# Kernel optimization log

Hardware: AMD Instinct MI355X
Metric: run time of the kernel (lower is better)

## Reference

```python
import jax, jax.numpy as jnp
import numpy as np

B, S, D, H = 2, 2048, 1024, 16
DH = D // H


def setup_inputs() -> dict:
    key = jax.random.key(0)
    ks = jax.random.split(key, 6)
    scale = 0.02
    X = jax.random.normal(ks[0], (B, S, D), dtype=jnp.float32)
    masks = jax.random.randint(ks[1], (B, S), 0, 2).astype(jnp.int32)
    Wq = jax.random.normal(ks[2], (D, D), dtype=jnp.float32) * scale
    Wk = jax.random.normal(ks[3], (D, D), dtype=jnp.float32) * scale
    Wv = jax.random.normal(ks[4], (D, D), dtype=jnp.float32) * scale
    Wo = jax.random.normal(ks[5], (D, D), dtype=jnp.float32) * scale
    return {"X": X, "masks": masks, "Wq": Wq, "Wk": Wk, "Wv": Wv, "Wo": Wo}


def reference(X, masks, Wq, Wk, Wv, Wo):
    b, s, d = X.shape
    masks_b = masks.astype(bool)                       # [B,S] key validity
    lookahead = jnp.triu(jnp.ones((s, s), dtype=bool), 1)  # [S,S] future positions
    pad = ~masks_b[:, None, :]                         # [B,1,S] -> invalid keys
    invalid = pad | lookahead[None, :, :]              # [B,S,S]
    valid = (~invalid)[:, None, :, :].astype(X.dtype)  # [B,1,S,S]

    def split_heads(Y):  # [B,S,D] -> [B,H,S,DH]
        return Y.reshape(b, s, H, DH).transpose(0, 2, 1, 3)

    Q = split_heads(X @ Wq.T)
    K = split_heads(X @ Wk.T)
    V = split_heads(X @ Wv.T)

    Qn = Q / jnp.sqrt(jnp.sum(Q * Q, axis=-1, keepdims=True))
    Kn = K / jnp.sqrt(jnp.sum(K * K, axis=-1, keepdims=True))

    scores = jnp.einsum('bhqd,bhkd->bhqk', Qn, Kn)     # cosine similarities
    att = jax.nn.relu(scores) * valid                  # relu + causal/pad mask
    ctx = jnp.einsum('bhqk,bhkd->bhqd', att, V)
    ctx = ctx * masks_b[:, None, :, None].astype(X.dtype)  # zero padded queries

    out = ctx.transpose(0, 2, 1, 3).reshape(b, s, d)
    return out @ Wo.T
```

## Files before the change

kernel.cpp:

```cpp
#include <hip/hip_runtime.h>
#include <hip/hip_bf16.h>

#define BB 2
#define SS 2048
#define DD 1024
#define HH 16
#define MMR (BB*SS)
#define ND3 3072

typedef __hip_bfloat16 bf;
typedef __bf16 bf16x8 __attribute__((ext_vector_type(8)));
typedef float f32x4 __attribute__((ext_vector_type(4)));
typedef float f32x16 __attribute__((ext_vector_type(16)));

#define VMCNT(n) asm volatile("s_waitcnt vmcnt(" #n ")" ::: "memory")

__device__ __forceinline__ f32x4 mfma16(bf16x8 a, bf16x8 b, f32x4 c) {
    return __builtin_amdgcn_mfma_f32_16x16x32_bf16(a, b, c, 0, 0, 0);
}
__device__ __forceinline__ f32x16 mfma32(bf16x8 a, bf16x8 b, f32x16 c) {
    return __builtin_amdgcn_mfma_f32_32x32x16_bf16(a, b, c, 0, 0, 0);
}
__device__ __forceinline__ unsigned cvt_pk_bf16(float lo, float hi) {
    unsigned r;
    asm("v_cvt_pk_bf16_f32 %0, %1, %2" : "=v"(r) : "v"(lo), "v"(hi));
    return r;
}
__device__ __forceinline__ void pl32swap(unsigned& a, unsigned& b) {
    asm("v_permlane32_swap_b32 %0, %1" : "+v"(a), "+v"(b));
}
__device__ __forceinline__ void glds16(const bf* g, bf* l) {
    __builtin_amdgcn_global_load_lds(
        (const __attribute__((address_space(1))) void*)g,
        (__attribute__((address_space(3))) void*)l,
        16, 0, 0);
}

__global__ __launch_bounds__(256) void k_convert(const float* __restrict__ X,
                                                 const float* __restrict__ Wq,
                                                 const float* __restrict__ Wk,
                                                 const float* __restrict__ Wv,
                                                 const float* __restrict__ Wo,
                                                 bf* __restrict__ Xb,
                                                 bf* __restrict__ Wqkv,
                                                 bf* __restrict__ Wob) {
    const int bid = blockIdx.x;
    const float* src;
    bf* dst;
    int off;
    if (bid < 4096) {
        src = X; dst = Xb; off = bid;
    } else {
        const int r = (bid - 4096) >> 10;
        src = (r == 0) ? Wq : (r == 1) ? Wk : (r == 2) ? Wv : Wo;
        dst = (r < 3) ? (Wqkv + (size_t)r * 1048576) : Wob;
        off = (bid - 4096) & 1023;
    }
    const int j = (off * 256 + threadIdx.x) * 4;
    float4 v = *(const float4*)(src + j);
    bf tmp[4];
    tmp[0] = __float2bfloat16(v.x);
    tmp[1] = __float2bfloat16(v.y);
    tmp[2] = __float2bfloat16(v.z);
    tmp[3] = __float2bfloat16(v.w);
    *(uint2*)(dst + j) = *(const uint2*)tmp;
}

__global__ __launch_bounds__(512, 6) void k_gemm8(const bf* __restrict__ A,
                                                  const bf* __restrict__ Bt,
                                                  const int* __restrict__ masks,
                                                  bf* __restrict__ Qn,
                                                  bf* __restrict__ Kn,
                                                  bf* __restrict__ Vt,
                                                  int nx, int K) {
    __shared__ __align__(16) bf Asm[3][128 * 32];
    __shared__ __align__(16) bf Bsm[3][128 * 32];
    const int tid = threadIdx.x;
    const int w = tid >> 6, lane = tid & 63, g = lane >> 4, rl = lane & 15;
    const int cpx = gridDim.x >> 3;
    const int swz = (blockIdx.x & 7) * cpx + (blockIdx.x >> 3);
    const int m0 = (swz / nx) * 128, n0 = (swz % nx) * 128;
    const int wr = (w >> 1) * 32, wc = (w & 1) * 64;
    const int lrow = lane >> 2, lseg = lane & 3;
    const int xseg = lseg ^ ((lrow >> 1) & 3);

    f32x4 acc[2][4] = {};
    const bf* Ap = A + (size_t)m0 * K;
    const bf* Bp = Bt + (size_t)n0 * K;

    auto stage = [&](int bi, int k0) {
        glds16(Ap + (size_t)(w * 16 + lrow) * K + k0 + xseg * 8, &Asm[bi][w * 512]);
        glds16(Bp + (size_t)(w * 16 + lrow) * K + k0 + xseg * 8, &Bsm[bi][w * 512]);
    };

    const int T = K >> 5;
    stage(0, 0);
    stage(1, 32);
    int cur = 0, nxt = 2;
    for (int t = 0; t < T; ++t) {
        __builtin_amdgcn_sched_barrier(0);
        if (t < T - 1) { VMCNT(2); } else { VMCNT(0); }
        __builtin_amdgcn_s_barrier();
        __builtin_amdgcn_sched_barrier(0);
        if (t + 2 < T) stage(nxt, (t + 2) * 32);

        const bf* Ab = Asm[cur];
        const bf* Bb = Bsm[cur];
        bf16x8 af[2], bfr[4];
#pragma unroll
        for (int m = 0; m < 2; ++m) {
            const int row = wr + m * 16 + rl;
            af[m] = __builtin_bit_cast(bf16x8,
                *(const int4*)&Ab[row * 32 + (g ^ ((row >> 1) & 3)) * 8]);
        }
#pragma unroll
        for (int n = 0; n < 4; ++n) {
            const int row = wc + n * 16 + rl;
            bfr[n] = __builtin_bit_cast(bf16x8,
                *(const int4*)&Bb[row * 32 + (g ^ ((row >> 1) & 3)) * 8]);
        }
        __builtin_amdgcn_s_setprio(1);
#pragma unroll
        for (int m = 0; m < 2; ++m)
#pragma unroll
            for (int n = 0; n < 4; ++n)
                acc[m][n] = mfma16(af[m], bfr[n], acc[m][n]);
        __builtin_amdgcn_s_setprio(0);

        cur = (cur == 2) ? 0 : cur + 1;
        nxt = (nxt == 2) ? 0 : nxt + 1;
    }

    const int ncol0 = n0 + wc;
    if (ncol0 < 2048) {
        bf* dst = (ncol0 < 1024) ? Qn : Kn;
        const int h2 = (ncol0 >> 6) & 15;
#pragma unroll
        for (int m = 0; m < 2; ++m) {
#pragma unroll
            for (int ri = 0; ri < 4; ++ri) {
                const int row = m0 + wr + m * 16 + g * 4 + ri;
                float ss = 0.f;
#pragma unroll
                for (int n = 0; n < 4; ++n) ss += acc[m][n][ri] * acc[m][n][ri];
#pragma unroll
                for (int d = 1; d < 16; d <<= 1) ss += __shfl_xor(ss, d, 64);
                const float sc = rsqrtf(ss) * (masks[row] ? 1.0f : 0.0f);
                const int b = row >> 11, s = row & 2047;
                const size_t base = ((size_t)(b * HH + h2) * SS + s) * 64;
#pragma unroll
                for (int n = 0; n < 4; ++n)
                    dst[base + n * 16 + rl] = __float2bfloat16(acc[m][n][ri] * sc);
            }
        }
    } else {
        const int h2 = (ncol0 - 2048) >> 6;
        const int b = (m0 + wr) >> 11;
        const int sb = ((m0 + wr) & 2047) + g * 4;
#pragma unroll
        for (int m = 0; m < 2; ++m)
#pragma unroll
            for (int n = 0; n < 4; ++n) {
                const int d = n * 16 + rl;
                bf t4[4];
#pragma unroll
                for (int ri = 0; ri < 4; ++ri) t4[ri] = __float2bfloat16(acc[m][n][ri]);
                *(uint2*)&Vt[((size_t)(b * HH + h2) * 64 + d) * SS + sb + m * 16] =
                    *(uint2*)t4;
            }
    }
}

__global__ __launch_bounds__(256) void k_gemm(const bf* __restrict__ A,
                                              const bf* __restrict__ Bt,
                                              float* __restrict__ Cf,
                                              int nx, int N, int K) {
    constexpr int BM = 64, BN = 128;
    __shared__ __align__(16) bf Asm[3][BM * 32];
    __shared__ __align__(16) bf Bsm[3][BN * 32];
    const int tid = threadIdx.x;
    const int w = tid >> 6, lane = tid & 63, g = lane >> 4, rl = lane & 15;
    const int cpx = gridDim.x >> 3;
    const int swz = (blockIdx.x & 7) * cpx + (blockIdx.x >> 3);
    const int m0 = (swz / nx) * BM, n0 = (swz % nx) * BN;
    const int wr = (w >> 1) * 32, wc = (w & 1) * 64;
    const int lrow = lane >> 2, lseg = lane & 3;
    const int xseg = lseg ^ ((lrow >> 1) & 3);

    f32x4 acc[2][4] = {};
    const bf* Ap = A + (size_t)m0 * K;
    const bf* Bp = Bt + (size_t)n0 * K;

    auto stage = [&](int bi, int k0) {
        glds16(Ap + (size_t)(w * 16 + lrow) * K + k0 + xseg * 8, &Asm[bi][w * 512]);
#pragma unroll
        for (int u = 0; u < 2; ++u)
            glds16(Bp + (size_t)(u * 64 + w * 16 + lrow) * K + k0 + xseg * 8,
                   &Bsm[bi][(u * 64 + w * 16) * 32]);
    };

    const int T = K >> 5;
    stage(0, 0);
    stage(1, 32);
    int cur = 0, nxt = 2;
    for (int t = 0; t < T; ++t) {
        __builtin_amdgcn_sched_barrier(0);
        if (t < T - 1) { VMCNT(3); } else { VMCNT(0); }
        __builtin_amdgcn_s_barrier();
        __builtin_amdgcn_sched_barrier(0);
        if (t + 2 < T) stage(nxt, (t + 2) * 32);

        const bf* Ab = Asm[cur];
        const bf* Bb = Bsm[cur];
        bf16x8 af[2], bfr[4];
#pragma unroll
        for (int m = 0; m < 2; ++m) {
            const int row = wr + m * 16 + rl;
            af[m] = __builtin_bit_cast(bf16x8,
                *(const int4*)&Ab[row * 32 + (g ^ ((row >> 1) & 3)) * 8]);
        }
#pragma unroll
        for (int n = 0; n < 4; ++n) {
            const int row = wc + n * 16 + rl;
            bfr[n] = __builtin_bit_cast(bf16x8,
                *(const int4*)&Bb[row * 32 + (g ^ ((row >> 1) & 3)) * 8]);
        }
        __builtin_amdgcn_s_setprio(1);
#pragma unroll
        for (int m = 0; m < 2; ++m)
#pragma unroll
            for (int n = 0; n < 4; ++n)
                acc[m][n] = mfma16(af[m], bfr[n], acc[m][n]);
        __builtin_amdgcn_s_setprio(0);

        cur = (cur == 2) ? 0 : cur + 1;
        nxt = (nxt == 2) ? 0 : nxt + 1;
    }

#pragma unroll
    for (int m = 0; m < 2; ++m)
#pragma unroll
        for (int n = 0; n < 4; ++n)
#pragma unroll
            for (int ri = 0; ri < 4; ++ri)
                Cf[(size_t)(m0 + wr + m * 16 + g * 4 + ri) * N + n0 + wc + n * 16 + rl] =
                    acc[m][n][ri];
}

__global__ __launch_bounds__(256) void k_attn(const bf* __restrict__ Qn,
                                              const bf* __restrict__ Kn,
                                              const bf* __restrict__ Vt,
                                              bf* __restrict__ Ctx) {
    __shared__ __align__(16) bf Ksm[2][64 * 64];
    __shared__ __align__(16) bf Vsm[2][64 * 64];

    const int idx = blockIdx.x;
    const int qt = 31 - (idx >> 5);
    const int by = idx & 31;
    const int b = by >> 4, h = by & 15;
    const int tid = threadIdx.x;
    const int w = tid >> 6, lane = tid & 63;
    const int l31 = lane & 31, hl = lane >> 5;
    const int qh = w >> 1;
    const int kp = w & 1;
    const int qw = qt * 64 + qh * 32;
    const int qg = qw + l31;

    const bf* Qp = Qn + (size_t)by * SS * 64;
    const bf* Kp = Kn + (size_t)by * SS * 64;
    const bf* Vp = Vt + (size_t)by * 64 * SS;

    bf16x8 aqs[4];
#pragma unroll
    for (int st = 0; st < 4; ++st)
        aqs[st] = __builtin_bit_cast(bf16x8,
            *(const int4*)(Qp + (size_t)(qw + l31) * 64 + st * 16 + hl * 8));

    const int srow = lane >> 3;
    const int sblk = (lane & 7) ^ srow;

    auto stage = [&](int buf, int k0) {
#pragma unroll
        for (int u = 0; u < 2; ++u) {
            const int c = w * 2 + u;
            const int row = c * 8 + srow;
            glds16(Kp + (size_t)(k0 + row) * 64 + sblk * 8, &Ksm[buf][c * 512]);
            glds16(Vp + (size_t)row * SS + k0 + sblk * 8, &Vsm[buf][c * 512]);
        }
    };

    f32x16 accd[2] = {};

    stage(0, 0);
    __syncthreads();
    int cur = 0;
    for (int t = 0; t <= qt; ++t) {
        if (t < qt) stage(cur ^ 1, (t + 1) * 64);
        const int kb = t * 64 + kp * 32;
        if (kb <= qw + 31) {
            f32x16 pc = {};
#pragma unroll
            for (int st = 0; st < 4; ++st) {
                const int r = kp * 32 + l31;
                bf16x8 ak = __builtin_bit_cast(bf16x8,
                    *(const int4*)&Ksm[cur][r * 64 + (((2 * st + hl) ^ (r & 7)) << 3)]);
                pc = mfma32(ak, aqs[st], pc);
            }
            const bool dg = (kb + 31 > qw);
            float pv[16];
#pragma unroll
            for (int m2 = 0; m2 < 16; ++m2) {
                float v = fmaxf(pc[m2], 0.0f);
                if (dg) {
                    const int kg = kb + (m2 & 3) + 8 * (m2 >> 2) + 4 * hl;
                    if (kg > qg) v = 0.0f;
                }
                pv[m2] = v;
            }
            unsigned P[8];
#pragma unroll
            for (int m2 = 0; m2 < 8; ++m2) P[m2] = cvt_pk_bf16(pv[2 * m2], pv[2 * m2 + 1]);
            pl32swap(P[0], P[2]);
            pl32swap(P[1], P[3]);
            pl32swap(P[4], P[6]);
            pl32swap(P[5], P[7]);
#pragma unroll
            for (int s = 0; s < 2; ++s) {
                uint4 pw = {P[4 * s + 0], P[4 * s + 1], P[4 * s + 2], P[4 * s + 3]};
                bf16x8 pa = __builtin_bit_cast(bf16x8, pw);
#pragma unroll
                for (int dt = 0; dt < 2; ++dt) {
                    const int d = dt * 32 + l31;
                    const int slot = kp * 4 + s * 2 + hl;
                    bf16x8 bv = __builtin_bit_cast(bf16x8,
                        *(const int4*)&Vsm[cur][d * 64 + ((slot ^ (d & 7)) << 3)]);
                    accd[dt] = mfma32(pa, bv, accd[dt]);
                }
            }
        }
        __syncthreads();
        cur ^= 1;
    }

    float* red = (float*)&Ksm[0][0];
    if (kp == 1) {
#pragma unroll
        for (int dt = 0; dt < 2; ++dt)
#pragma unroll
            for (int m2 = 0; m2 < 16; ++m2)
                red[qh * 2048 + (dt * 16 + m2) * 64 + lane] = accd[dt][m2];
    }
    __syncthreads();
    if (kp == 0) {
#pragma unroll
        for (int dt = 0; dt < 2; ++dt)
#pragma unroll
            for (int m2 = 0; m2 < 16; ++m2) {
                const float v = accd[dt][m2] + red[qh * 2048 + (dt * 16 + m2) * 64 + lane];
                const int q = qw + (m2 & 3) + 8 * (m2 >> 2) + 4 * hl;
                const int d = dt * 32 + l31;
                Ctx[(size_t)(b * SS + q) * DD + h * 64 + d] = __float2bfloat16(v);
            }
    }
}

extern "C" void kernel_launch(void* const* d_in, const int* in_sizes, int n_in,
                              void* d_out, int out_size, void* d_ws, size_t ws_size,
                              hipStream_t stream) {
    const float* X  = (const float*)d_in[0];
    const int* masks = (const int*)d_in[1];
    const float* Wq = (const float*)d_in[2];
    const float* Wk = (const float*)d_in[3];
    const float* Wv = (const float*)d_in[4];
    const float* Wo = (const float*)d_in[5];
    float* out = (float*)d_out;
    char* ws = (char*)d_ws;

    const size_t MB = 1024 * 1024;
    bf* Xb   = (bf*)(ws);
    bf* Wqkv = (bf*)(ws + 8  * MB);
    bf* Wob  = (bf*)(ws + 14 * MB);
    bf* Qn   = (bf*)(ws + 16 * MB);
    bf* Kn   = (bf*)(ws + 24 * MB);
    bf* Vt   = (bf*)(ws + 32 * MB);
    bf* Ctx  = (bf*)(ws + 40 * MB);

    k_convert<<<8192, 256, 0, stream>>>(X, Wq, Wk, Wv, Wo, Xb, Wqkv, Wob);

    k_gemm8<<<(ND3 / 128) * (MMR / 128), 512, 0, stream>>>(
        Xb, Wqkv, masks, Qn, Kn, Vt, ND3 / 128, DD);

    k_attn<<<1024, 256, 0, stream>>>(Qn, Kn, Vt, Ctx);

    k_gemm<<<(DD / 128) * (MMR / 64), 256, 0, stream>>>(
        Ctx, Wob, out, DD / 128, DD, DD);
}
```

Measured before the change: 102.5 us.

## Pair causal query tiles per attention block to balance work and share K/V

Each attention block now handles two query tiles, j and 31-j, so every block does the same causal work, and one staged K/V tile serves both. The grid is halved to 512 blocks with an XCD-style block index swizzle. The aim is to remove the tail imbalance of causal tiles and halve K/V global and LDS traffic per query. In exchange register pressure roughly doubles (two Q fragment sets and two accumulator sets), which may lower occupancy, and there are fewer blocks to fill the GPU.

```diff
diff --git a/kernel.cpp b/kernel.cpp
--- a/kernel.cpp
+++ b/kernel.cpp
@@ -251,30 +251,34 @@
                                               const bf* __restrict__ Kn,
                                               const bf* __restrict__ Vt,
                                               bf* __restrict__ Ctx) {
-    __shared__ __align__(16) bf Ksm[2][64 * 64];
-    __shared__ __align__(16) bf Vsm[2][64 * 64];
-
-    const int idx = blockIdx.x;
-    const int qt = 31 - (idx >> 5);
-    const int by = idx & 31;
+    __shared__ __align__(16) bf smem[16384];
+    bf* Ksm = smem;
+    bf* Vsm = smem + 8192;
+
+    const int swz = (blockIdx.x & 7) * 64 + (blockIdx.x >> 3);
+    const int by = swz >> 4;
+    const int j  = swz & 15;
     const int b = by >> 4, h = by & 15;
     const int tid = threadIdx.x;
     const int w = tid >> 6, lane = tid & 63;
     const int l31 = lane & 31, hl = lane >> 5;
     const int qh = w >> 1;
     const int kp = w & 1;
-    const int qw = qt * 64 + qh * 32;
-    const int qg = qw + l31;
+    const int qA = j * 64 + qh * 32;
+    const int qB = (31 - j) * 64 + qh * 32;
 
     const bf* Qp = Qn + (size_t)by * SS * 64;
     const bf* Kp = Kn + (size_t)by * SS * 64;
     const bf* Vp = Vt + (size_t)by * 64 * SS;
 
-    bf16x8 aqs[4];
-#pragma unroll
-    for (int st = 0; st < 4; ++st)
-        aqs[st] = __builtin_bit_cast(bf16x8,
-            *(const int4*)(Qp + (size_t)(qw + l31) * 64 + st * 16 + hl * 8));
+    bf16x8 aqsA[4], aqsB[4];
+#pragma unroll
+    for (int st = 0; st < 4; ++st) {
+        aqsA[st] = __builtin_bit_cast(bf16x8,
+            *(const int4*)(Qp + (size_t)(qA + l31) * 64 + st * 16 + hl * 8));
+        aqsB[st] = __builtin_bit_cast(bf16x8,
+            *(const int4*)(Qp + (size_t)(qB + l31) * 64 + st * 16 + hl * 8));
+    }
 
     const int srow = lane >> 3;
     const int sblk = (lane & 7) ^ srow;
@@ -284,71 +288,86 @@
         for (int u = 0; u < 2; ++u) {
             const int c = w * 2 + u;
             const int row = c * 8 + srow;
-            glds16(Kp + (size_t)(k0 + row) * 64 + sblk * 8, &Ksm[buf][c * 512]);
-            glds16(Vp + (size_t)row * SS + k0 + sblk * 8, &Vsm[buf][c * 512]);
+            glds16(Kp + (size_t)(k0 + row) * 64 + sblk * 8, &Ksm[buf * 4096 + c * 512]);
+            glds16(Vp + (size_t)row * SS + k0 + sblk * 8, &Vsm[buf * 4096 + c * 512]);
         }
     };
 
-    f32x16 accd[2] = {};
+    auto packP = [&](const f32x16& pc, int qgBase, int kb, bf16x8 (&pa)[2]) {
+        const bool dg = (kb + 31 > qgBase);
+        float pv[16];
+#pragma unroll
+        for (int m2 = 0; m2 < 16; ++m2) {
+            float v = fmaxf(pc[m2], 0.0f);
+            if (dg) {
+                const int kg = kb + (m2 & 3) + 8 * (m2 >> 2) + 4 * hl;
+                if (kg > qgBase + l31) v = 0.0f;
+            }
+            pv[m2] = v;
+        }
+        unsigned P[8];
+#pragma unroll
+        for (int m2 = 0; m2 < 8; ++m2) P[m2] = cvt_pk_bf16(pv[2 * m2], pv[2 * m2 + 1]);
+        pl32swap(P[0], P[2]); pl32swap(P[1], P[3]);
+        pl32swap(P[4], P[6]); pl32swap(P[5], P[7]);
+        uint4 w0 = {P[0], P[1], P[2], P[3]}, w1 = {P[4], P[5], P[6], P[7]};
+        pa[0] = __builtin_bit_cast(bf16x8, w0);
+        pa[1] = __builtin_bit_cast(bf16x8, w1);
+    };
+
+    f32x16 accA[2] = {}, accB[2] = {};
+    const int T = 32 - j;
 
     stage(0, 0);
     __syncthreads();
     int cur = 0;
-    for (int t = 0; t <= qt; ++t) {
-        if (t < qt) stage(cur ^ 1, (t + 1) * 64);
+    for (int t = 0; t < T; ++t) {
+        if (t + 1 < T) stage(cur ^ 1, (t + 1) * 64);
         const int kb = t * 64 + kp * 32;
-        if (kb <= qw + 31) {
-            f32x16 pc = {};
+        const bool needA = (kb <= qA + 31);
+        const bool needB = (kb <= qB + 31);
+        if (needB || needA) {
+            const bf* Ks = &Ksm[cur * 4096];
+            const bf* Vs = &Vsm[cur * 4096];
+            const int r = kp * 32 + l31;
+            f32x16 pcA = {}, pcB = {};
 #pragma unroll
             for (int st = 0; st < 4; ++st) {
-                const int r = kp * 32 + l31;
                 bf16x8 ak = __builtin_bit_cast(bf16x8,
-                    *(const int4*)&Ksm[cur][r * 64 + (((2 * st + hl) ^ (r & 7)) << 3)]);
-                pc = mfma32(ak, aqs[st], pc);
-            }
-            const bool dg = (kb + 31 > qw);
-            float pv[16];
-#pragma unroll
-            for (int m2 = 0; m2 < 16; ++m2) {
-                float v = fmaxf(pc[m2], 0.0f);
-                if (dg) {
-                    const int kg = kb + (m2 & 3) + 8 * (m2 >> 2) + 4 * hl;
-                    if (kg > qg) v = 0.0f;
-                }
-                pv[m2] = v;
-            }
-            unsigned P[8];
-#pragma unroll
-            for (int m2 = 0; m2 < 8; ++m2) P[m2] = cvt_pk_bf16(pv[2 * m2], pv[2 * m2 + 1]);
-            pl32swap(P[0], P[2]);
-            pl32swap(P[1], P[3]);
-            pl32swap(P[4], P[6]);
-            pl32swap(P[5], P[7]);
-#pragma unroll
-            for (int s = 0; s < 2; ++s) {
-                uint4 pw = {P[4 * s + 0], P[4 * s + 1], P[4 * s + 2], P[4 * s + 3]};
-                bf16x8 pa = __builtin_bit_cast(bf16x8, pw);
+                    *(const int4*)&Ks[r * 64 + (((2 * st + hl) ^ (r & 7)) << 3)]);
+                if (needA) pcA = mfma32(ak, aqsA[st], pcA);
+                if (needB) pcB = mfma32(ak, aqsB[st], pcB);
+            }
+            bf16x8 paA[2], paB[2];
+            if (needA) packP(pcA, qA, kb, paA);
+            if (needB) packP(pcB, qB, kb, paB);
+#pragma unroll
+            for (int s = 0; s < 2; ++s)
 #pragma unroll
                 for (int dt = 0; dt < 2; ++dt) {
                     const int d = dt * 32 + l31;
                     const int slot = kp * 4 + s * 2 + hl;
                     bf16x8 bv = __builtin_bit_cast(bf16x8,
-                        *(const int4*)&Vsm[cur][d * 64 + ((slot ^ (d & 7)) << 3)]);
-                    accd[dt] = mfma32(pa, bv, accd[dt]);
+                        *(const int4*)&Vs[d * 64 + ((slot ^ (d & 7)) << 3)]);
+                    if (needA) accA[dt] = mfma32(paA[s], bv, accA[dt]);
+                    if (needB) accB[dt] = mfma32(paB[s], bv, accB[dt]);
                 }
-            }
         }
         __syncthreads();
         cur ^= 1;
     }
 
-    float* red = (float*)&Ksm[0][0];
+    float* red = (float*)smem;
     if (kp == 1) {
 #pragma unroll
         for (int dt = 0; dt < 2; ++dt)
 #pragma unroll
-            for (int m2 = 0; m2 < 16; ++m2)
-                red[qh * 2048 + (dt * 16 + m2) * 64 + lane] = accd[dt][m2];
+            for (int m2 = 0; m2 < 16; ++m2) {
+                const int crow = (m2 & 3) + 8 * (m2 >> 2) + 4 * hl;
+                const int d = dt * 32 + l31;
+                red[(qh * 32 + crow) * 64 + d] = accA[dt][m2];
+                red[(64 + qh * 32 + crow) * 64 + d] = accB[dt][m2];
+            }
     }
     __syncthreads();
     if (kp == 0) {
@@ -356,10 +375,12 @@
         for (int dt = 0; dt < 2; ++dt)
 #pragma unroll
             for (int m2 = 0; m2 < 16; ++m2) {
-                const float v = accd[dt][m2] + red[qh * 2048 + (dt * 16 + m2) * 64 + lane];
-                const int q = qw + (m2 & 3) + 8 * (m2 >> 2) + 4 * hl;
+                const int crow = (m2 & 3) + 8 * (m2 >> 2) + 4 * hl;
                 const int d = dt * 32 + l31;
-                Ctx[(size_t)(b * SS + q) * DD + h * 64 + d] = __float2bfloat16(v);
+                const float vA = accA[dt][m2] + red[(qh * 32 + crow) * 64 + d];
+                const float vB = accB[dt][m2] + red[(64 + qh * 32 + crow) * 64 + d];
+                Ctx[(size_t)(b * SS + qA + crow) * DD + h * 64 + d] = __float2bfloat16(vA);
+                Ctx[(size_t)(b * SS + qB + crow) * DD + h * 64 + d] = __float2bfloat16(vB);
             }
     }
 }
@@ -390,7 +411,7 @@
     k_gemm8<<<(ND3 / 128) * (MMR / 128), 512, 0, stream>>>(
         Xb, Wqkv, masks, Qn, Kn, Vt, ND3 / 128, DD);
 
-    k_attn<<<1024, 256, 0, stream>>>(Qn, Kn, Vt, Ctx);
+    k_attn<<<512, 256, 0, stream>>>(Qn, Kn, Vt, Ctx);
 
     k_gemm<<<(DD / 128) * (MMR / 64), 256, 0, stream>>>(
         Ctx, Wob, out, DD / 128, DD, DD);
```

Result: slower. 166.4 us (+62.4%).
